# Kernel optimization log

Hardware: AMD Instinct MI355X
Metric: run time of the kernel (lower is better)

## Reference

```python
import jax, jax.numpy as jnp
import numpy as np


def _softsplat(inp, flow):
    # inp: [N,C,H,W], flow: [N,2,H,W] -> bilinear forward splat via 4 scatter-adds
    n, c, h, w = inp.shape
    hw = h * w
    yy, xx = jnp.meshgrid(jnp.arange(h, dtype=inp.dtype), jnp.arange(w, dtype=inp.dtype), indexing='ij')
    xx = xx[None] + flow[:, 0]  # [N,H,W] target x coords
    yy = yy[None] + flow[:, 1]  # [N,H,W] target y coords
    x0 = jnp.floor(xx); y0 = jnp.floor(yy)
    x1 = x0 + 1.0;      y1 = y0 + 1.0
    corners = (
        (x0, y0, (x1 - xx) * (y1 - yy)),
        (x1, y0, (xx - x0) * (y1 - yy)),
        (x0, y1, (x1 - xx) * (yy - y0)),
        (x1, y1, (xx - x0) * (yy - y0)),
    )
    batch_off = (jnp.arange(n, dtype=jnp.int32) * hw)[:, None, None]  # [N,1,1]
    vals_base = inp.transpose(1, 0, 2, 3)  # [C,N,H,W]
    out = jnp.zeros((c, n * hw), dtype=inp.dtype)
    for xi, yi, wgt in corners:  # fixed 4-way unroll
        xl = xi.astype(jnp.int32)
        yl = yi.astype(jnp.int32)
        valid = (xl >= 0) & (xl < w) & (yl >= 0) & (yl < h)
        lin = jnp.clip(yl, 0, h - 1) * w + jnp.clip(xl, 0, w - 1) + batch_off  # [N,H,W]
        wv = wgt * valid.astype(inp.dtype)  # [N,H,W]
        vals = (vals_base * wv[None]).reshape(c, -1)  # [C, N*H*W]
        out = out.at[:, lin.reshape(-1)].add(vals)
    return out.reshape(c, n, h, w).transpose(1, 0, 2, 3)


def setup_inputs() -> dict:
    key = jax.random.key(0)
    k1, k2, k3 = jax.random.split(key, 3)
    tenInput = jax.random.normal(k1, (4, 64, 256, 448), dtype=jnp.float32)
    tenFlow = jax.random.normal(k2, (4, 2, 256, 448), dtype=jnp.float32) * 4.0
    tenMetric = jax.random.normal(k3, (4, 1, 256, 448), dtype=jnp.float32)
    return {"tenInput": tenInput, "tenFlow": tenFlow, "tenMetric": tenMetric}


def reference(tenInput, tenFlow, tenMetric):
    # strType == 'softmax'
    metric = jnp.exp(tenMetric)  # [N,1,H,W]
    inp = jnp.concatenate([tenInput * metric, metric], axis=1)  # [N,C+1,H,W]
    out = _softsplat(inp, tenFlow)
    norm = out[:, -1:]
    norm = jnp.where(norm == 0.0, jnp.ones_like(norm), norm)
    return out[:, :-1] / norm
```

## Files before the change

kernel.cpp:

```cpp
#include <hip/hip_runtime.h>

#define NB 4
#define CH 64
#define HH 256
#define WW 448
constexpr int HW     = HH * WW;
constexpr int NPIX   = NB * HW;
constexpr int NROWS  = NB * HH;
constexpr int NTILE  = NPIX / 64;
constexpr int ROWCAP = 1536;
constexpr int FCAP   = 2 * ROWCAP;

constexpr size_t CNT_OFF  = 1024;
constexpr size_t OFF_OFF  = CNT_OFF + (size_t)NPIX;
constexpr size_t CE_OFF   = OFF_OFF + (size_t)NPIX;
constexpr size_t FE_OFF   = CE_OFF + (size_t)NROWS * ROWCAP * 4;
constexpr size_t TINP_OFF = FE_OFF + (size_t)NROWS * FCAP * 2;

__device__ __forceinline__ unsigned int bf16rne(float f) {
    unsigned int u = __float_as_uint(f);
    return (u + 0x7FFFu + ((u >> 16) & 1u)) >> 16;
}

__global__ __launch_bounds__(256) void pass_a(
    const float* __restrict__ inp, const float* __restrict__ flow,
    const float* __restrict__ metric,
    unsigned int* __restrict__ tinp, int* __restrict__ row_counts,
    int4* __restrict__ centries)
{
    __shared__ float tile[64][CH + 1];
    __shared__ float sfx[64], sfy[64], sm[64];
    __shared__ int whist[64], wbase[64];

    int b   = blockIdx.x;
    int blk = (b & 7) * (NTILE / 8) + (b >> 3);
    int nb    = blk / (HW / 64);
    int tpix0 = (blk - nb * (HW / 64)) * 64;
    int t = threadIdx.x;

    if (t < 64)        sfx[t]       = flow[(nb * 2 + 0) * HW + tpix0 + t];
    else if (t < 128)  sfy[t - 64]  = flow[(nb * 2 + 1) * HW + tpix0 + (t - 64)];
    else if (t < 192)  sm[t - 128]  = expf(metric[nb * HW + tpix0 + (t - 128)]);
    else               whist[t - 192] = 0;

    int p  = t & 63;
    int c0 = (t >> 6) * 16;
    const float* ip = inp + (size_t)nb * CH * HW + tpix0 + p;
    #pragma unroll
    for (int cc = 0; cc < 16; ++cc)
        tile[p][c0 + cc] = ip[(size_t)(c0 + cc) * HW];

    __syncthreads();

    int y     = tpix0 / WW;
    int xbase = tpix0 - y * WW;

    bool emit = false;
    int  bin = -1, lrank = 0, rglob = -1, srcp = 0, x0c = 0;
    float wl = 0.0f, wr = 0.0f;

    if (t < 128) {
        int pl = t & 63, rsel = t >> 6;
        float fx = sfx[pl], fy = sfy[pl], m = sm[pl];
        float yy  = (float)y + fy;
        float y0f = floorf(yy);
        int   yr  = (int)y0f + rsel;
        float wyr = rsel ? (yy - y0f) : (1.0f - (yy - y0f));
        int   xq  = xbase + pl;
        float xx  = (float)xq + fx;
        float x0f = floorf(xx);
        int   x0  = (int)x0f;
        float wxf = xx - x0f;

        if (yr >= 0 && yr < HH && x0 >= -1 && x0 <= WW - 1) {
            emit = true;
            srcp = nb * HW + y * WW + xq;
            wl = (1.0f - wxf) * wyr * m;
            wr = wxf * wyr * m;
            if (x0 < 0)            { x0c = 0;      wl = wr;  wr = 0.0f; }
            else if (x0 == WW - 1) { x0c = WW - 2; wr = wl;  wl = 0.0f; }
            else                   { x0c = x0; }
            rglob = nb * HH + yr;
            bin = yr - (y - 30);
            if (bin >= 0 && bin < 64) lrank = atomicAdd(&whist[bin], 1);
            else bin = -1;
        }
    }
    __syncthreads();

    if (t < 64 && whist[t] > 0)
        wbase[t] = atomicAdd(&row_counts[nb * HH + (y - 30) + t], whist[t]);
    __syncthreads();

    if (emit) {
        int rank = (bin >= 0) ? (wbase[bin] + lrank)
                              : atomicAdd(&row_counts[rglob], 1);
        if (rank < ROWCAP)
            centries[(size_t)rglob * ROWCAP + rank] =
                make_int4(srcp, x0c, __float_as_int(wl), __float_as_int(wr));
    }

    int q  = t >> 2;
    int cb = (t & 3) * 16;
    unsigned int pk[8];
    #pragma unroll
    for (int j = 0; j < 8; ++j) {
        unsigned int lo = bf16rne(tile[q][cb + 2 * j]);
        unsigned int hi = bf16rne(tile[q][cb + 2 * j + 1]);
        pk[j] = lo | (hi << 16);
    }
    unsigned int* op = tinp + (size_t)(nb * HW + tpix0 + q) * 32 + (cb >> 1);
    *reinterpret_cast<uint4*>(op)     = make_uint4(pk[0], pk[1], pk[2], pk[3]);
    *reinterpret_cast<uint4*>(op + 4) = make_uint4(pk[4], pk[5], pk[6], pk[7]);
}

__global__ __launch_bounds__(256) void pass_c(
    const int* __restrict__ row_counts, const int4* __restrict__ centries,
    int* __restrict__ counts, int* __restrict__ offs, int2* __restrict__ fentries)
{
    __shared__ int4 ce[ROWCAP];
    __shared__ int hist[512];
    __shared__ int pstart[512];
    __shared__ int cur[WW];
    __shared__ int tmp[256];

    int r   = blockIdx.x;
    int tid = threadIdx.x;
    int nE  = row_counts[r];
    if (nE > ROWCAP) nE = ROWCAP;

    for (int e = tid; e < nE; e += 256) ce[e] = centries[(size_t)r * ROWCAP + e];
    for (int i = tid; i < 512; i += 256) hist[i] = 0;
    __syncthreads();

    for (int e = tid; e < nE; e += 256) {
        int x0 = ce[e].y;
        atomicAdd(&hist[x0], 1);
        atomicAdd(&hist[x0 + 1], 1);
    }
    __syncthreads();

    int a0 = hist[2 * tid], a1 = hist[2 * tid + 1];
    int s = a0 + a1;
    tmp[tid] = s;
    __syncthreads();
    int val = s;
    for (int d = 1; d < 256; d <<= 1) {
        int xv = (tid >= d) ? tmp[tid - d] : 0;
        __syncthreads();
        val += xv;
        tmp[tid] = val;
        __syncthreads();
    }
    int ex = val - s;
    pstart[2 * tid]     = ex;
    pstart[2 * tid + 1] = ex + a0;
    __syncthreads();

    int nbq = r / HH, yq = r - nbq * HH;
    size_t tb = (size_t)nbq * HW + (size_t)yq * WW;
    int rowbase = r * FCAP;
    for (int x = tid; x < WW; x += 256) {
        counts[tb + x] = hist[x];
        offs[tb + x]   = rowbase + pstart[x];
        cur[x] = pstart[x];
    }
    __syncthreads();

    for (int e = tid; e < nE; e += 256) {
        int4 en = ce[e];
        int x0 = en.y;
        int rkL = atomicAdd(&cur[x0], 1);
        int rkR = atomicAdd(&cur[x0 + 1], 1);
        fentries[rowbase + rkL] = make_int2(en.x, en.z);
        fentries[rowbase + rkR] = make_int2(en.x, en.w);
    }
}

__device__ __forceinline__ void bfma2(float& alo, float& ahi, float w, unsigned int u) {
    alo = fmaf(w, __uint_as_float(u << 16), alo);
    ahi = fmaf(w, __uint_as_float(u & 0xFFFF0000u), ahi);
}

__global__ __launch_bounds__(448) void gather_row(
    const uint4* __restrict__ tinp, const int* __restrict__ row_counts,
    const int* __restrict__ counts, const int* __restrict__ offs,
    const int2* __restrict__ fentries, float* __restrict__ out)
{
    __shared__ int2 eb[FCAP];

    int b = blockIdx.x;
    int r = (b & 7) * (NROWS / 8) + (b >> 3);
    int tid = threadIdx.x;

    int rowbase = r * FCAP;
    int tot = row_counts[r] * 2;
    if (tot > FCAP) tot = FCAP;
    for (int e = tid; e < tot; e += 448) eb[e] = fentries[rowbase + e];

    int nbq = r / HH, yq = r - nbq * HH;
    int t = nbq * HW + yq * WW + tid;
    int k  = counts[t];
    int mo = offs[t] - rowbase;
    __syncthreads();

    float ksum = 0.0f;
    for (int e = 0; e < k; ++e) ksum += __int_as_float(eb[mo + e].y);
    float rn = (ksum == 0.0f) ? 1.0f : 1.0f / ksum;

    size_t tbase = (size_t)nbq * CH * HW + (size_t)yq * WW + tid;

    #pragma unroll
    for (int g = 0; g < 4; ++g) {
        float a[16];
        #pragma unroll
        for (int j = 0; j < 16; ++j) a[j] = 0.0f;

        for (int e = 0; e < k; ++e) {
            int2 en = eb[mo + e];
            float w = __int_as_float(en.y);
            size_t bi = (size_t)en.x * 8 + g * 2;
            uint4 v0 = tinp[bi];
            uint4 v1 = tinp[bi + 1];
            bfma2(a[0],  a[1],  w, v0.x);
            bfma2(a[2],  a[3],  w, v0.y);
            bfma2(a[4],  a[5],  w, v0.z);
            bfma2(a[6],  a[7],  w, v0.w);
            bfma2(a[8],  a[9],  w, v1.x);
            bfma2(a[10], a[11], w, v1.y);
            bfma2(a[12], a[13], w, v1.z);
            bfma2(a[14], a[15], w, v1.w);
        }
        float* ob = out + tbase + (size_t)(g * 16) * HW;
        #pragma unroll
        for (int j = 0; j < 16; ++j)
            __builtin_nontemporal_store(a[j] * rn, ob + (size_t)j * HW);
    }
}

extern "C" void kernel_launch(void* const* d_in, const int* in_sizes, int n_in,
                              void* d_out, int out_size, void* d_ws, size_t ws_size,
                              hipStream_t stream) {
    const float* tenInput  = (const float*)d_in[0];
    const float* tenFlow   = (const float*)d_in[1];
    const float* tenMetric = (const float*)d_in[2];
    float* out = (float*)d_out;

    int*          row_counts = (int*)d_ws;
    int*          counts     = row_counts + CNT_OFF;
    int*          offs       = row_counts + OFF_OFF;
    int4*         centries   = (int4*)(row_counts + CE_OFF);
    int2*         fentries   = (int2*)(row_counts + FE_OFF);
    unsigned int* tinp       = (unsigned int*)(row_counts + TINP_OFF);

    hipMemsetAsync(row_counts, 0, NROWS * sizeof(int), stream);

    pass_a<<<NTILE, 256, 0, stream>>>(tenInput, tenFlow, tenMetric,
                                      tinp, row_counts, centries);
    pass_c<<<NROWS, 256, 0, stream>>>(row_counts, centries, counts, offs, fentries);
    gather_row<<<NROWS, 448, 0, stream>>>((const uint4*)tinp, row_counts,
                                          counts, offs, fentries, out);
}
```

Baseline: 281.3 us.

## Fuse row bucketing and gather into one quarter-row kernel with wave-cooperative channel gather

Merges the per-row counting-sort pass and the gather pass into a single kernel. Each block handles a quarter of an output row, builds its bucket list in shared memory, and lets each wavefront gather one destination pixel at a time, with lanes spread across channels and two entries processed per step. Results are staged in a shared tile so the transposed output can be written with coalesced nontemporal stores. This removes one launch and the global round-trip of counts, offsets and sorted entries. In exchange every quarter-row block rescans the whole row's candidate list, and the per-pixel loop is serial within each wavefront.

```diff
diff --git a/kernel.cpp b/kernel.cpp
--- a/kernel.cpp
+++ b/kernel.cpp
@@ -9,13 +9,11 @@
 constexpr int NROWS  = NB * HH;
 constexpr int NTILE  = NPIX / 64;
 constexpr int ROWCAP = 1536;
-constexpr int FCAP   = 2 * ROWCAP;
-
-constexpr size_t CNT_OFF  = 1024;
-constexpr size_t OFF_OFF  = CNT_OFF + (size_t)NPIX;
-constexpr size_t CE_OFF   = OFF_OFF + (size_t)NPIX;
-constexpr size_t FE_OFF   = CE_OFF + (size_t)NROWS * ROWCAP * 4;
-constexpr size_t TINP_OFF = FE_OFF + (size_t)NROWS * FCAP * 2;
+constexpr int QW     = 112;
+constexpr int EBC    = 1536;
+
+constexpr size_t CE_OFF   = 1024;
+constexpr size_t TINP_OFF = CE_OFF + (size_t)NROWS * ROWCAP * 4;
 
 __device__ __forceinline__ unsigned int bf16rne(float f) {
     unsigned int u = __float_as_uint(f);
@@ -114,127 +112,101 @@
     *reinterpret_cast<uint4*>(op + 4) = make_uint4(pk[4], pk[5], pk[6], pk[7]);
 }
 
-__global__ __launch_bounds__(256) void pass_c(
-    const int* __restrict__ row_counts, const int4* __restrict__ centries,
-    int* __restrict__ counts, int* __restrict__ offs, int2* __restrict__ fentries)
+__global__ __launch_bounds__(256) void pass_bc(
+    const unsigned int* __restrict__ tinp, const int* __restrict__ row_counts,
+    const int4* __restrict__ centries, float* __restrict__ out)
 {
-    __shared__ int4 ce[ROWCAP];
-    __shared__ int hist[512];
-    __shared__ int pstart[512];
-    __shared__ int cur[WW];
-    __shared__ int tmp[256];
-
-    int r   = blockIdx.x;
+    __shared__ float acc[QW][CH + 1];
+    __shared__ int2  eb[EBC];
+    __shared__ int   hist[QW], pstart[QW], cur[QW];
+    __shared__ int   tmp[128];
+
+    int b   = blockIdx.x;
+    int qd  = b & 3;
+    int r   = b >> 2;
+    int xlo = qd * QW;
     int tid = threadIdx.x;
-    int nE  = row_counts[r];
+
+    int nE = row_counts[r];
     if (nE > ROWCAP) nE = ROWCAP;
-
-    for (int e = tid; e < nE; e += 256) ce[e] = centries[(size_t)r * ROWCAP + e];
-    for (int i = tid; i < 512; i += 256) hist[i] = 0;
+    size_t rowbase = (size_t)r * ROWCAP;
+
+    for (int i = tid; i < QW; i += 256) hist[i] = 0;
     __syncthreads();
 
     for (int e = tid; e < nE; e += 256) {
-        int x0 = ce[e].y;
-        atomicAdd(&hist[x0], 1);
-        atomicAdd(&hist[x0 + 1], 1);
-    }
-    __syncthreads();
-
-    int a0 = hist[2 * tid], a1 = hist[2 * tid + 1];
-    int s = a0 + a1;
-    tmp[tid] = s;
-    __syncthreads();
-    int val = s;
-    for (int d = 1; d < 256; d <<= 1) {
-        int xv = (tid >= d) ? tmp[tid - d] : 0;
+        int x0 = centries[rowbase + e].y;
+        int a = x0 - xlo, bx = x0 + 1 - xlo;
+        if (a  >= 0 && a  < QW) atomicAdd(&hist[a], 1);
+        if (bx >= 0 && bx < QW) atomicAdd(&hist[bx], 1);
+    }
+    __syncthreads();
+
+    if (tid < 128) tmp[tid] = (tid < QW) ? hist[tid] : 0;
+    __syncthreads();
+    for (int d = 1; d < 128; d <<= 1) {
+        int v = 0;
+        if (tid < 128) { v = tmp[tid]; if (tid >= d) v += tmp[tid - d]; }
         __syncthreads();
-        val += xv;
-        tmp[tid] = val;
+        if (tid < 128) tmp[tid] = v;
         __syncthreads();
     }
-    int ex = val - s;
-    pstart[2 * tid]     = ex;
-    pstart[2 * tid + 1] = ex + a0;
+    if (tid < QW) { pstart[tid] = tmp[tid] - hist[tid]; cur[tid] = tmp[tid] - hist[tid]; }
+    __syncthreads();
+
+    for (int e = tid; e < nE; e += 256) {
+        int4 en = centries[rowbase + e];
+        int a = en.y - xlo, bx = en.y + 1 - xlo;
+        if (a >= 0 && a < QW) {
+            int s = atomicAdd(&cur[a], 1);
+            if (s < EBC) eb[s] = make_int2(en.x, en.z);
+        }
+        if (bx >= 0 && bx < QW) {
+            int s = atomicAdd(&cur[bx], 1);
+            if (s < EBC) eb[s] = make_int2(en.x, en.w);
+        }
+    }
+    __syncthreads();
+
+    int lane = tid & 63;
+    int wid  = tid >> 6;
+    int chp  = lane & 31;
+    int half = lane >> 5;
+
+    for (int i = 0; i < QW / 4; ++i) {
+        int px = wid * (QW / 4) + i;
+        int kk = hist[px];
+        int mo = pstart[px];
+
+        float a0 = 0.0f, a1 = 0.0f, ws = 0.0f;
+        for (int e = 0; e < kk; e += 2) {
+            int ei = e + half;
+            bool v = ei < kk;
+            int2 en = eb[mo + (v ? ei : 0)];
+            float w = v ? __int_as_float(en.y) : 0.0f;
+            unsigned int u = tinp[(size_t)en.x * 32 + chp];
+            a0 = fmaf(w, __uint_as_float(u << 16), a0);
+            a1 = fmaf(w, __uint_as_float(u & 0xFFFF0000u), a1);
+            ws += w;
+        }
+        a0 += __shfl_xor(a0, 32);
+        a1 += __shfl_xor(a1, 32);
+        ws += __shfl_xor(ws, 32);
+        float rn = (ws == 0.0f) ? 1.0f : 1.0f / ws;
+        if (half == 0) {
+            acc[px][2 * chp]     = a0 * rn;
+            acc[px][2 * chp + 1] = a1 * rn;
+        }
+    }
     __syncthreads();
 
     int nbq = r / HH, yq = r - nbq * HH;
-    size_t tb = (size_t)nbq * HW + (size_t)yq * WW;
-    int rowbase = r * FCAP;
-    for (int x = tid; x < WW; x += 256) {
-        counts[tb + x] = hist[x];
-        offs[tb + x]   = rowbase + pstart[x];
-        cur[x] = pstart[x];
-    }
-    __syncthreads();
-
-    for (int e = tid; e < nE; e += 256) {
-        int4 en = ce[e];
-        int x0 = en.y;
-        int rkL = atomicAdd(&cur[x0], 1);
-        int rkR = atomicAdd(&cur[x0 + 1], 1);
-        fentries[rowbase + rkL] = make_int2(en.x, en.z);
-        fentries[rowbase + rkR] = make_int2(en.x, en.w);
-    }
-}
-
-__device__ __forceinline__ void bfma2(float& alo, float& ahi, float w, unsigned int u) {
-    alo = fmaf(w, __uint_as_float(u << 16), alo);
-    ahi = fmaf(w, __uint_as_float(u & 0xFFFF0000u), ahi);
-}
-
-__global__ __launch_bounds__(448) void gather_row(
-    const uint4* __restrict__ tinp, const int* __restrict__ row_counts,
-    const int* __restrict__ counts, const int* __restrict__ offs,
-    const int2* __restrict__ fentries, float* __restrict__ out)
-{
-    __shared__ int2 eb[FCAP];
-
-    int b = blockIdx.x;
-    int r = (b & 7) * (NROWS / 8) + (b >> 3);
-    int tid = threadIdx.x;
-
-    int rowbase = r * FCAP;
-    int tot = row_counts[r] * 2;
-    if (tot > FCAP) tot = FCAP;
-    for (int e = tid; e < tot; e += 448) eb[e] = fentries[rowbase + e];
-
-    int nbq = r / HH, yq = r - nbq * HH;
-    int t = nbq * HW + yq * WW + tid;
-    int k  = counts[t];
-    int mo = offs[t] - rowbase;
-    __syncthreads();
-
-    float ksum = 0.0f;
-    for (int e = 0; e < k; ++e) ksum += __int_as_float(eb[mo + e].y);
-    float rn = (ksum == 0.0f) ? 1.0f : 1.0f / ksum;
-
-    size_t tbase = (size_t)nbq * CH * HW + (size_t)yq * WW + tid;
-
-    #pragma unroll
-    for (int g = 0; g < 4; ++g) {
-        float a[16];
-        #pragma unroll
-        for (int j = 0; j < 16; ++j) a[j] = 0.0f;
-
-        for (int e = 0; e < k; ++e) {
-            int2 en = eb[mo + e];
-            float w = __int_as_float(en.y);
-            size_t bi = (size_t)en.x * 8 + g * 2;
-            uint4 v0 = tinp[bi];
-            uint4 v1 = tinp[bi + 1];
-            bfma2(a[0],  a[1],  w, v0.x);
-            bfma2(a[2],  a[3],  w, v0.y);
-            bfma2(a[4],  a[5],  w, v0.z);
-            bfma2(a[6],  a[7],  w, v0.w);
-            bfma2(a[8],  a[9],  w, v1.x);
-            bfma2(a[10], a[11], w, v1.y);
-            bfma2(a[12], a[13], w, v1.z);
-            bfma2(a[14], a[15], w, v1.w);
-        }
-        float* ob = out + tbase + (size_t)(g * 16) * HW;
-        #pragma unroll
-        for (int j = 0; j < 16; ++j)
-            __builtin_nontemporal_store(a[j] * rn, ob + (size_t)j * HW);
+    float* ob = out + (size_t)nbq * CH * HW + (size_t)yq * WW + xlo;
+    for (int j = 0; j < (QW * CH) / 256; ++j) {
+        int lin = j * 256 + tid;
+        int c  = lin / QW;
+        int px = lin - c * QW;
+        __builtin_nontemporal_store(acc[px][c], ob + (size_t)c * HW + px);
     }
 }
 
@@ -247,17 +219,12 @@
     float* out = (float*)d_out;
 
     int*          row_counts = (int*)d_ws;
-    int*          counts     = row_counts + CNT_OFF;
-    int*          offs       = row_counts + OFF_OFF;
     int4*         centries   = (int4*)(row_counts + CE_OFF);
-    int2*         fentries   = (int2*)(row_counts + FE_OFF);
     unsigned int* tinp       = (unsigned int*)(row_counts + TINP_OFF);
 
     hipMemsetAsync(row_counts, 0, NROWS * sizeof(int), stream);
 
     pass_a<<<NTILE, 256, 0, stream>>>(tenInput, tenFlow, tenMetric,
                                       tinp, row_counts, centries);
-    pass_c<<<NROWS, 256, 0, stream>>>(row_counts, centries, counts, offs, fentries);
-    gather_row<<<NROWS, 448, 0, stream>>>((const uint4*)tinp, row_counts,
-                                          counts, offs, fentries, out);
-}
+    pass_bc<<<NROWS * 4, 256, 0, stream>>>(tinp, row_counts, centries, out);
+}
```

Result: slower. 397.2 us (+41.2%).
